# Optimization experiments

Hardware: AMD Instinct MI355X
Metric: run time of the kernel (lower is better)

The kernel has to match this reference:

```python
import jax, jax.numpy as jnp
import numpy as np

N = 100000   # nodes
E = 600000   # edges
B = 512      # graphs in batch
H = 128      # hidden dim
ED = 8       # edge feature dim
TWO48 = float(2 ** 48 - 1)


def _w(k, shape, fan_in):
    return jax.random.normal(k, shape, jnp.float32) * (1.0 / np.sqrt(fan_in))


def setup_inputs() -> dict:
    key = jax.random.key(0)
    ks = jax.random.split(key, 32)
    inp = {}
    inp["s_node_ids"] = jax.random.randint(ks[0], (N,), 0, 2 ** 31 - 1, dtype=jnp.int32)
    inp["s_edge_index"] = jax.random.randint(ks[1], (2, E), 0, N, dtype=jnp.int32)
    inp["s_edge_attr"] = jax.random.normal(ks[2], (E, ED), jnp.float32)
    inp["s_batch"] = jnp.sort(jax.random.randint(ks[3], (N,), 0, B, dtype=jnp.int32))
    inp["depth"] = jax.random.uniform(ks[4], (B,), jnp.float32)
    # id_mlp: Linear(1,H) -> ReLU -> Linear(H,H)
    inp["id_w1"] = _w(ks[5], (1, H), 1); inp["id_b1"] = jnp.zeros((H,), jnp.float32)
    inp["id_w2"] = _w(ks[6], (H, H), H); inp["id_b2"] = jnp.zeros((H,), jnp.float32)
    # edge_mlp: Linear(ED,H) -> ReLU -> Linear(H,H)
    inp["ed_w1"] = _w(ks[7], (ED, H), ED); inp["ed_b1"] = jnp.zeros((H,), jnp.float32)
    inp["ed_w2"] = _w(ks[8], (H, H), H); inp["ed_b2"] = jnp.zeros((H,), jnp.float32)
    # GINEConv nn MLPs: Linear(H,H) -> ReLU -> Linear(H,H)
    inp["c1_w1"] = _w(ks[9], (H, H), H); inp["c1_b1"] = jnp.zeros((H,), jnp.float32)
    inp["c1_w2"] = _w(ks[10], (H, H), H); inp["c1_b2"] = jnp.zeros((H,), jnp.float32)
    inp["c2_w1"] = _w(ks[11], (H, H), H); inp["c2_b1"] = jnp.zeros((H,), jnp.float32)
    inp["c2_w2"] = _w(ks[12], (H, H), H); inp["c2_b2"] = jnp.zeros((H,), jnp.float32)
    inp["rg_w1"] = _w(ks[13], (H + 1, H), H + 1); inp["rg_b1"] = jnp.zeros((H,), jnp.float32)
    inp["rg_w2"] = _w(ks[14], (H, 1), H); inp["rg_b2"] = jnp.zeros((1,), jnp.float32)
    return inp


def _mlp2(x, w1, b1, w2, b2):
    return jax.nn.relu(x @ w1 + b1) @ w2 + b2


def _gine(x, src, dst, e, w1, b1, w2, b2):
    # message = ReLU(x_j + e), sum-aggregated at dst; out = nn((1+eps)*x + aggr), eps=0
    msg = jax.nn.relu(x[src] + e)                       # [E, H]
    aggr = jax.ops.segment_sum(msg, dst, num_segments=N)  # [N, H]
    return _mlp2(x + aggr, w1, b1, w2, b2)


def _global_mean(x, batch):
    sums = jax.ops.segment_sum(x, batch, num_segments=B)                          # [B, H]
    cnts = jax.ops.segment_sum(jnp.ones((x.shape[0], 1), x.dtype), batch, num_segments=B)
    return sums / jnp.maximum(cnts, 1.0)


def reference(s_node_ids, s_edge_index, s_edge_attr, s_batch, depth,
              id_w1, id_b1, id_w2, id_b2,
              ed_w1, ed_b1, ed_w2, ed_b2,
              c1_w1, c1_b1, c1_w2, c1_b2,
              c2_w1, c2_b1, c2_w2, c2_b2,
              rg_w1, rg_b1, rg_w2, rg_b2):
    src, dst = s_edge_index[0], s_edge_index[1]
    x0 = jnp.clip(s_node_ids.astype(jnp.float32) / TWO48, 0.0, 1.0)[:, None]  # [N,1]
    x = _mlp2(x0, id_w1, id_b1, id_w2, id_b2)                                 # [N,H]
    e = _mlp2(s_edge_attr, ed_w1, ed_b1, ed_w2, ed_b2)                        # [E,H]
    x = jax.nn.relu(_gine(x, src, dst, e, c1_w1, c1_b1, c1_w2, c1_b2))
    x = jax.nn.relu(_gine(x, src, dst, e, c2_w1, c2_b1, c2_w2, c2_b2))
    rep = jnp.concatenate([_global_mean(x, s_batch), depth[:, None]], axis=1)  # [B,H+1]
    return _mlp2(rep, rg_w1, rg_b1, rg_w2, rg_b2)[:, 0]                        # [B]
```

## Files before the change

kernel.cpp:

```cpp
#include <hip/hip_runtime.h>
#include <hip/hip_bf16.h>

#define N_NODES 100000
#define N_EDGES 600000
#define NB      512
#define H       128
#define ED      8
#define SCAN_CHUNK 1024
#define N_CHUNKS   98
#define EDGE_BLKS  3125
#define NODE_TILES 1563

typedef __attribute__((ext_vector_type(8))) short short8;
typedef __attribute__((ext_vector_type(4))) float f32x4;
typedef __attribute__((ext_vector_type(4))) unsigned int u32x4;
typedef unsigned short u16;
typedef unsigned int   u32;

static __device__ __forceinline__ u16 f2bf(float f) {
    u32 u = __float_as_uint(f);
    u32 r = u + 0x7fffu + ((u >> 16) & 1u);
    return (u16)(r >> 16);
}
static __device__ __forceinline__ float bf2f(u32 h) {
    return __uint_as_float(h << 16);
}
static __device__ __forceinline__ u32 bfpack(float lo, float hi) {
    u32 r;
    asm("v_cvt_pk_bf16_f32 %0, %1, %2" : "=v"(r) : "v"(lo), "v"(hi));
    return r;
}

__global__ __launch_bounds__(256) void pack_hist_kernel(
    const float* __restrict__ W0, const float* __restrict__ W1,
    const float* __restrict__ W2, const float* __restrict__ W3,
    const float* __restrict__ W4, const float* __restrict__ W5,
    const float* __restrict__ W6,
    short8* __restrict__ O0, short8* __restrict__ O1,
    short8* __restrict__ O2, short8* __restrict__ O3,
    short8* __restrict__ O4, short8* __restrict__ O5,
    short8* __restrict__ O6,
    const int* __restrict__ edge_index, int* __restrict__ counts,
    uint4* __restrict__ sums_zero)
{
    const int HIST_BLKS = (N_EDGES + 255) / 256;
    if (blockIdx.x >= 50 + HIST_BLKS) {
        int idx = (blockIdx.x - 50 - HIST_BLKS) * 256 + threadIdx.x;
        if (idx < 16384) sums_zero[idx] = make_uint4(0, 0, 0, 0);
        return;
    }
    if (blockIdx.x >= 50) {
        int e = (blockIdx.x - 50) * 256 + threadIdx.x;
        if (e < N_EDGES) atomicAdd(&counts[edge_index[N_EDGES + e]], 1);
        return;
    }
    int gid = blockIdx.x * 256 + threadIdx.x;
    const float* W; short8* O; int Krows, kkmax, slot;
    if (gid < 512) { W = W0; O = O0; Krows = ED; kkmax = 1; slot = gid; }
    else {
        int m = (gid - 512) / 2048;
        slot = (gid - 512) % 2048;
        Krows = H; kkmax = 4;
        switch (m) {
            case 0: W = W1; O = O1; break;
            case 1: W = W2; O = O2; break;
            case 2: W = W3; O = O3; break;
            case 3: W = W4; O = O4; break;
            case 4: W = W5; O = O5; break;
            default: W = W6; O = O6; break;
        }
    }
    int lane = slot & 63;
    int t = slot >> 6;
    int nt = t & 1; t >>= 1;
    int kk = t % kkmax;
    int w  = t / kkmax;
    int quad = lane >> 4, n15 = lane & 15;
    int n = w * 32 + nt * 16 + n15;
    short8 v;
    #pragma unroll
    for (int j = 0; j < 8; j++) {
        int k = kk * 32 + quad * 8 + j;
        v[j] = (k < Krows) ? (short)f2bf(W[k * H + n]) : (short)0;
    }
    O[slot] = v;
}

__global__ __launch_bounds__(256) void scan_kernel(
    const int* __restrict__ counts, int* __restrict__ chunk_scan,
    int* __restrict__ bsum_raw)
{
    __shared__ int sS[256];
    int tid = threadIdx.x;
    int base = blockIdx.x * SCAN_CHUNK + tid * 4;
    int4 v = *(const int4*)&counts[base];
    int q0 = v.x, q1 = q0 + v.y, q2 = q1 + v.z, q3 = q2 + v.w;
    sS[tid] = q3;
    __syncthreads();
    #pragma unroll
    for (int off = 1; off < 256; off <<= 1) {
        int t = (tid >= off) ? sS[tid - off] : 0;
        __syncthreads();
        sS[tid] += t;
        __syncthreads();
    }
    int excl = sS[tid] - q3;
    int4 o;
    o.x = excl; o.y = excl + q0; o.z = excl + q1; o.w = excl + q2;
    *(int4*)&chunk_scan[base] = o;
    if (tid == 255) bsum_raw[blockIdx.x] = sS[255];
}

__global__ __launch_bounds__(256) void fill_kernel(
    const int* __restrict__ edge_index,
    const int* __restrict__ chunk_scan, const int* __restrict__ bsum_raw,
    int* __restrict__ counts, int* __restrict__ src_list,
    const float* __restrict__ attr, u16* __restrict__ attr_perm)
{
    __shared__ int sB[128];
    int tid = threadIdx.x;
    int v0 = 0;
    if (tid < 128) {
        v0 = (tid < N_CHUNKS) ? bsum_raw[tid] : 0;
        sB[tid] = v0;
    }
    __syncthreads();
    #pragma unroll
    for (int off = 1; off < 128; off <<= 1) {
        int t = (tid < 128 && tid >= off) ? sB[tid - off] : 0;
        __syncthreads();
        if (tid < 128) sB[tid] += t;
        __syncthreads();
    }
    if (tid < 128) sB[tid] -= v0;
    __syncthreads();

    int e = blockIdx.x * 256 + tid;
    if (e >= N_EDGES) return;
    int src = edge_index[e];
    int dst = edge_index[N_EDGES + e];
    int slot = atomicAdd(&counts[dst], -1) - 1;
    int pos = chunk_scan[dst] + sB[dst >> 10] + slot;
    src_list[pos] = src;
    float4 a0 = *(const float4*)&attr[(long)e * ED];
    float4 a1 = *(const float4*)&attr[(long)e * ED + 4];
    u32 w0 = bfpack(a0.x, a0.y);
    u32 w1 = bfpack(a0.z, a0.w);
    u32 w2 = bfpack(a1.x, a1.y);
    u32 w3 = bfpack(a1.z, a1.w);
    *(uint4*)&attr_perm[(long)pos * ED] = make_uint4(w0, w1, w2, w3);
}

__global__ __launch_bounds__(256) void edge_node_mfma(
    const u16* __restrict__ attr_perm,
    const int* __restrict__ chunk_scan, const int* __restrict__ bsum_raw,
    int* __restrict__ row_start,
    const short8* __restrict__ pW1, const float* __restrict__ b1,
    const short8* __restrict__ pW2, const float* __restrict__ b2,
    u16* __restrict__ e_perm,
    const int* __restrict__ ids,
    const float* __restrict__ id_w1, const float* __restrict__ id_b1,
    const short8* __restrict__ id_pW2, const float* __restrict__ id_b2,
    u16* __restrict__ x_out)
{
    __shared__ u16 sH[64 * 136];
    __shared__ int sB[128];
    __shared__ float s_x0[64];
    int tid = threadIdx.x;

    if (blockIdx.x >= EDGE_BLKS) {
        int tile = blockIdx.x - EDGE_BLKS;
        int w = tid >> 6, lane = tid & 63, quad = lane >> 4, n15 = lane & 15;
        short8 fW2[4][2];
        #pragma unroll
        for (int kk = 0; kk < 4; kk++) {
            fW2[kk][0] = id_pW2[((w * 4 + kk) * 2 + 0) * 64 + lane];
            fW2[kk][1] = id_pW2[((w * 4 + kk) * 2 + 1) * 64 + lane];
        }
        float rb2[2] = { id_b2[w * 32 + n15], id_b2[w * 32 + 16 + n15] };
        float w1c = id_w1[tid & 127], b1c = id_b1[tid & 127];
        int row0 = tile * 64;
        if (tid < 64) {
            int n = row0 + tid;
            float x0 = (n < N_NODES) ? (float)ids[n] / 281474976710655.0f : 0.0f;
            s_x0[tid] = fminf(fmaxf(x0, 0.0f), 1.0f);
        }
        __syncthreads();
        int half = tid >> 7, c = tid & 127;
        #pragma unroll
        for (int rr = 0; rr < 32; rr += 2) {
            int r = half + rr * 2;
            u32 p = bfpack(fmaxf(s_x0[r] * w1c + b1c, 0.0f),
                           fmaxf(s_x0[r + 2] * w1c + b1c, 0.0f));
            sH[r * 136 + c]       = (u16)p;
            sH[(r + 2) * 136 + c] = (u16)(p >> 16);
        }
        __syncthreads();
        f32x4 acc[4][2];
        #pragma unroll
        for (int s = 0; s < 4; s++) { acc[s][0] = (f32x4){0,0,0,0}; acc[s][1] = (f32x4){0,0,0,0}; }
        #pragma unroll
        for (int kk = 0; kk < 4; kk++) {
            #pragma unroll
            for (int s = 0; s < 4; s++) {
                short8 a = *(const short8*)&sH[(s * 16 + n15) * 136 + kk * 32 + quad * 8];
                acc[s][0] = __builtin_amdgcn_mfma_f32_16x16x32_bf16(a, fW2[kk][0], acc[s][0], 0, 0, 0);
                acc[s][1] = __builtin_amdgcn_mfma_f32_16x16x32_bf16(a, fW2[kk][1], acc[s][1], 0, 0, 0);
            }
        }
        __syncthreads();
        #pragma unroll
        for (int s = 0; s < 4; s++)
            #pragma unroll
            for (int nt = 0; nt < 2; nt++) {
                int col = w * 32 + nt * 16 + n15;
                int rb = (s * 16 + quad * 4) * 136 + col;
                u32 p0 = bfpack(acc[s][nt][0] + rb2[nt], acc[s][nt][1] + rb2[nt]);
                u32 p1 = bfpack(acc[s][nt][2] + rb2[nt], acc[s][nt][3] + rb2[nt]);
                sH[rb]       = (u16)p0;
                sH[rb + 136] = (u16)(p0 >> 16);
                sH[rb + 272] = (u16)p1;
                sH[rb + 408] = (u16)(p1 >> 16);
            }
        __syncthreads();
        for (int idx = tid; idx < 64 * 16; idx += 256) {
            int r = idx >> 4, c8 = (idx & 15) << 3;
            int n = row0 + r;
            if (n < N_NODES)
                *(uint4*)&x_out[(long)n * H + c8] = *(const uint4*)&sH[r * 136 + c8];
        }
        return;
    }

    if (blockIdx.x < 392) {
        int v0 = 0;
        if (tid < 128) {
            v0 = (tid < N_CHUNKS) ? bsum_raw[tid] : 0;
            sB[tid] = v0;
        }
        __syncthreads();
        #pragma unroll
        for (int off = 1; off < 128; off <<= 1) {
            int t = (tid < 128 && tid >= off) ? sB[tid - off] : 0;
            __syncthreads();
            if (tid < 128) sB[tid] += t;
            __syncthreads();
        }
        if (tid < 128) sB[tid] -= v0;
        __syncthreads();
        int i = blockIdx.x * 256 + tid;
        if (i <= N_NODES) row_start[i] = chunk_scan[i] + sB[i >> 10];
        __syncthreads();
    }

    int w = tid >> 6, lane = tid & 63, quad = lane >> 4, n15 = lane & 15;
    short8 fW1[2];
    fW1[0] = pW1[(w * 2 + 0) * 64 + lane];
    fW1[1] = pW1[(w * 2 + 1) * 64 + lane];
    short8 fW2[4][2];
    #pragma unroll
    for (int kk = 0; kk < 4; kk++) {
        fW2[kk][0] = pW2[((w * 4 + kk) * 2 + 0) * 64 + lane];
        fW2[kk][1] = pW2[((w * 4 + kk) * 2 + 1) * 64 + lane];
    }
    float rb1[2] = { b1[w * 32 + n15], b1[w * 32 + 16 + n15] };
    float rb2[2] = { b2[w * 32 + n15], b2[w * 32 + 16 + n15] };
    const short8 zero8 = (short8){0,0,0,0,0,0,0,0};
    const int ntile = N_EDGES / 64;
    for (int tile = blockIdx.x; tile < ntile; tile += EDGE_BLKS) {
        int row0 = tile * 64;
        short8 av[4];
        #pragma unroll
        for (int s = 0; s < 4; s++) {
            av[s] = zero8;
            if (quad == 0)
                av[s] = *(const short8*)&attr_perm[(long)(row0 + s * 16 + n15) * ED];
        }
        f32x4 acc[4][2];
        #pragma unroll
        for (int s = 0; s < 4; s++) { acc[s][0] = (f32x4){0,0,0,0}; acc[s][1] = (f32x4){0,0,0,0}; }
        #pragma unroll
        for (int s = 0; s < 4; s++) {
            acc[s][0] = __builtin_amdgcn_mfma_f32_16x16x32_bf16(av[s], fW1[0], acc[s][0], 0, 0, 0);
            acc[s][1] = __builtin_amdgcn_mfma_f32_16x16x32_bf16(av[s], fW1[1], acc[s][1], 0, 0, 0);
        }
        #pragma unroll
        for (int s = 0; s < 4; s++)
            #pragma unroll
            for (int nt = 0; nt < 2; nt++) {
                int col = w * 32 + nt * 16 + n15;
                int rb = (s * 16 + quad * 4) * 136 + col;
                u32 p0 = bfpack(fmaxf(acc[s][nt][0] + rb1[nt], 0.0f),
                                fmaxf(acc[s][nt][1] + rb1[nt], 0.0f));
                u32 p1 = bfpack(fmaxf(acc[s][nt][2] + rb1[nt], 0.0f),
                                fmaxf(acc[s][nt][3] + rb1[nt], 0.0f));
                sH[rb]       = (u16)p0;
                sH[rb + 136] = (u16)(p0 >> 16);
                sH[rb + 272] = (u16)p1;
                sH[rb + 408] = (u16)(p1 >> 16);
            }
        __syncthreads();
        #pragma unroll
        for (int s = 0; s < 4; s++) { acc[s][0] = (f32x4){0,0,0,0}; acc[s][1] = (f32x4){0,0,0,0}; }
        #pragma unroll
        for (int kk = 0; kk < 4; kk++) {
            #pragma unroll
            for (int s = 0; s < 4; s++) {
                short8 a = *(const short8*)&sH[(s * 16 + n15) * 136 + kk * 32 + quad * 8];
                acc[s][0] = __builtin_amdgcn_mfma_f32_16x16x32_bf16(a, fW2[kk][0], acc[s][0], 0, 0, 0);
                acc[s][1] = __builtin_amdgcn_mfma_f32_16x16x32_bf16(a, fW2[kk][1], acc[s][1], 0, 0, 0);
            }
        }
        __syncthreads();
        #pragma unroll
        for (int s = 0; s < 4; s++)
            #pragma unroll
            for (int nt = 0; nt < 2; nt++) {
                int col = w * 32 + nt * 16 + n15;
                int rb = (s * 16 + quad * 4) * 136 + col;
                u32 p0 = bfpack(acc[s][nt][0] + rb2[nt], acc[s][nt][1] + rb2[nt]);
                u32 p1 = bfpack(acc[s][nt][2] + rb2[nt], acc[s][nt][3] + rb2[nt]);
                sH[rb]       = (u16)p0;
                sH[rb + 136] = (u16)(p0 >> 16);
                sH[rb + 272] = (u16)p1;
                sH[rb + 408] = (u16)(p1 >> 16);
            }
        __syncthreads();
        for (int idx = tid; idx < 64 * 16; idx += 256) {
            int r = idx >> 4, c8 = (idx & 15) << 3;
            *(uint4*)&e_perm[(long)(row0 + r) * H + c8] = *(const uint4*)&sH[r * 136 + c8];
        }
        __syncthreads();
    }
}

static __device__ __forceinline__ void acc8(float* a, u32x4 xv, u32x4 ev) {
    #pragma unroll
    for (int q = 0; q < 4; q++) {
        a[2 * q + 0] += fmaxf(bf2f(xv[q] & 0xffff) + bf2f(ev[q] & 0xffff), 0.0f);
        a[2 * q + 1] += fmaxf(bf2f(xv[q] >> 16)    + bf2f(ev[q] >> 16),    0.0f);
    }
}

__global__ __launch_bounds__(256) void gine_fused(
    const int* __restrict__ row_start,
    const int* __restrict__ src_list,
    const u16* __restrict__ e_perm,
    const u16* __restrict__ x,
    const short8* __restrict__ pW1, const float* __restrict__ b1,
    const short8* __restrict__ pW2, const float* __restrict__ b2,
    u16* __restrict__ x_out,
    const int* __restrict__ batch,
    float* __restrict__ sums,
    float* __restrict__ part_sums,
    int* __restrict__ part_id,
    int do_pool)
{
    __shared__ u16 sA[16 * 136];
    __shared__ int sBt[16];
    int tid  = threadIdx.x;
    int lane = tid & 63;
    int l16  = lane & 15;
    int base = lane & 48;
    int fo   = l16 * 8;
    int r    = tid >> 4;
    int n    = blockIdx.x * 16 + r;
    const u16* xb = x + fo;

    if (do_pool && tid < 16) sBt[tid] = batch[blockIdx.x * 16 + tid];

    int beg = row_start[n];
    int end = row_start[n + 1];
    float a[8], b[8];
    #pragma unroll
    for (int q = 0; q < 8; q++) { a[q] = 0.0f; b[q] = 0.0f; }

    for (int j0 = beg; j0 < end; j0 += 16) {
        int m = min(16, end - j0);
        int sv = src_list[j0 + min(l16, m - 1)];
        const u16* ej = e_perm + (long)j0 * H + fo;
        int j = 0;
        for (; j + 2 <= m; j += 2) {
            int s0 = __shfl(sv, base | j);
            int s1 = __shfl(sv, base | (j + 1));
            u32x4 xv0 = *(const u32x4*)(xb + (long)s0 * H);
            u32x4 ev0 = *(const u32x4*)(ej + (long)(j + 0) * H);
            u32x4 xv1 = *(const u32x4*)(xb + (long)s1 * H);
            u32x4 ev1 = *(const u32x4*)(ej + (long)(j + 1) * H);
            acc8(a, xv0, ev0);
            acc8(b, xv1, ev1);
        }
        if (j < m) {
            int s0 = __shfl(sv, base | j);
            u32x4 xv0 = *(const u32x4*)(xb + (long)s0 * H);
            u32x4 ev0 = *(const u32x4*)(ej + (long)j * H);
            acc8(a, xv0, ev0);
        }
    }
    u32x4 xself = *(const u32x4*)(xb + (long)n * H);
    u32x4 xsrow;
    #pragma unroll
    for (int q = 0; q < 4; q++) {
        float o0 = bf2f(xself[q] & 0xffff) + a[2 * q + 0] + b[2 * q + 0];
        float o1 = bf2f(xself[q] >> 16)    + a[2 * q + 1] + b[2 * q + 1];
        xsrow[q] = bfpack(o0, o1);
    }
    *(uint4*)&sA[r * 136 + fo] = *(uint4*)&xsrow;
    __syncthreads();

    int w = tid >> 6, quad = lane >> 4, n15 = l16;
    float rb1[2] = { b1[w * 32 + n15], b1[w * 32 + 16 + n15] };
    float rb2[2] = { b2[w * 32 + n15], b2[w * 32 + 16 + n15] };
    f32x4 acc[2];
    acc[0] = (f32x4){0,0,0,0}; acc[1] = (f32x4){0,0,0,0};
    #pragma unroll
    for (int kk = 0; kk < 4; kk++) {
        short8 av = *(const short8*)&sA[n15 * 136 + kk * 32 + quad * 8];
        short8 w0 = pW1[((w * 4 + kk) * 2 + 0) * 64 + lane];
        short8 w1v = pW1[((w * 4 + kk) * 2 + 1) * 64 + lane];
        acc[0] = __builtin_amdgcn_mfma_f32_16x16x32_bf16(av, w0, acc[0], 0, 0, 0);
        acc[1] = __builtin_amdgcn_mfma_f32_16x16x32_bf16(av, w1v, acc[1], 0, 0, 0);
    }
    __syncthreads();
    #pragma unroll
    for (int nt = 0; nt < 2; nt++) {
        int col = w * 32 + nt * 16 + n15;
        int rb = (quad * 4) * 136 + col;
        u32 p0 = bfpack(fmaxf(acc[nt][0] + rb1[nt], 0.0f),
                        fmaxf(acc[nt][1] + rb1[nt], 0.0f));
        u32 p1 = bfpack(fmaxf(acc[nt][2] + rb1[nt], 0.0f),
                        fmaxf(acc[nt][3] + rb1[nt], 0.0f));
        sA[rb]       = (u16)p0;
        sA[rb + 136] = (u16)(p0 >> 16);
        sA[rb + 272] = (u16)p1;
        sA[rb + 408] = (u16)(p1 >> 16);
    }
    __syncthreads();
    acc[0] = (f32x4){0,0,0,0}; acc[1] = (f32x4){0,0,0,0};
    #pragma unroll
    for (int kk = 0; kk < 4; kk++) {
        short8 av = *(const short8*)&sA[n15 * 136 + kk * 32 + quad * 8];
        short8 w0 = pW2[((w * 4 + kk) * 2 + 0) * 64 + lane];
        short8 w1v = pW2[((w * 4 + kk) * 2 + 1) * 64 + lane];
        acc[0] = __builtin_amdgcn_mfma_f32_16x16x32_bf16(av, w0, acc[0], 0, 0, 0);
        acc[1] = __builtin_amdgcn_mfma_f32_16x16x32_bf16(av, w1v, acc[1], 0, 0, 0);
    }
    __syncthreads();
    #pragma unroll
    for (int nt = 0; nt < 2; nt++) {
        int col = w * 32 + nt * 16 + n15;
        int rb = (quad * 4) * 136 + col;
        u32 p0 = bfpack(fmaxf(acc[nt][0] + rb2[nt], 0.0f),
                        fmaxf(acc[nt][1] + rb2[nt], 0.0f));
        u32 p1 = bfpack(fmaxf(acc[nt][2] + rb2[nt], 0.0f),
                        fmaxf(acc[nt][3] + rb2[nt], 0.0f));
        sA[rb]       = (u16)p0;
        sA[rb + 136] = (u16)(p0 >> 16);
        sA[rb + 272] = (u16)p1;
        sA[rb + 408] = (u16)(p1 >> 16);
    }
    __syncthreads();
    if (!do_pool) {
        int rr = tid >> 4, c8 = (tid & 15) << 3;
        int nn = blockIdx.x * 16 + rr;
        *(uint4*)&x_out[(long)nn * H + c8] = *(const uint4*)&sA[rr * 136 + c8];
    } else {
        if (tid < 64) {
            int c2 = tid * 2;
            float s0 = 0.0f, s1 = 0.0f;
            int cur = sBt[0];
            int seg = 0;
            #pragma unroll
            for (int rr = 0; rr < 16; rr++) {
                int bb = sBt[rr];
                if (bb != cur) {
                    if (seg < 4) {
                        long pb = ((long)blockIdx.x * 4 + seg) * H;
                        part_sums[pb + c2]     = s0;
                        part_sums[pb + c2 + 1] = s1;
                    } else {
                        atomicAdd(&sums[cur * H + c2],     s0);
                        atomicAdd(&sums[cur * H + c2 + 1], s1);
                    }
                    s0 = s1 = 0.0f; cur = bb; seg++;
                }
                u32 v = *(const u32*)&sA[rr * 136 + c2];
                s0 += bf2f(v & 0xffff);
                s1 += bf2f(v >> 16);
            }
            if (seg < 4) {
                long pb = ((long)blockIdx.x * 4 + seg) * H;
                part_sums[pb + c2]     = s0;
                part_sums[pb + c2 + 1] = s1;
            } else {
                atomicAdd(&sums[cur * H + c2],     s0);
                atomicAdd(&sums[cur * H + c2 + 1], s1);
            }
        } else if (tid == 64) {
            int cur = sBt[0];
            int seg = 0;
            #pragma unroll
            for (int rr = 0; rr < 16; rr++) {
                int bb = sBt[rr];
                if (bb != cur) {
                    if (seg < 4) part_id[blockIdx.x * 4 + seg] = cur;
                    cur = bb; seg++;
                }
            }
            if (seg < 4) part_id[blockIdx.x * 4 + seg] = cur;
            for (int s2 = seg + 1; s2 < 4; s2++) part_id[blockIdx.x * 4 + s2] = -1;
        }
    }
}

__global__ __launch_bounds__(128) void regressor_kernel(
    const float* __restrict__ sums,
    const float* __restrict__ part_sums,
    const int* __restrict__ part_id,
    const int* __restrict__ batch,
    const float* __restrict__ depth,
    const float* __restrict__ w1, const float* __restrict__ b1,
    const float* __restrict__ w2, const float* __restrict__ b2,
    float* __restrict__ out)
{
    __shared__ float s_mean[H];
    __shared__ float s_red[2];
    int b = blockIdx.x;
    int j = threadIdx.x;
    int lo = 0, hi = N_NODES;
    while (lo < hi) { int mid = (lo + hi) >> 1; if (batch[mid] < b) lo = mid + 1; else hi = mid; }
    int n_start = lo;
    hi = N_NODES;
    while (lo < hi) { int mid = (lo + hi) >> 1; if (batch[mid] < b + 1) lo = mid + 1; else hi = mid; }
    int n_end = lo;
    float acc = sums[b * H + j];
    if (n_end > n_start) {
        int blk0 = n_start >> 4, blk1 = (n_end - 1) >> 4;
        for (int blk = blk0; blk <= blk1; blk++) {
            #pragma unroll
            for (int s = 0; s < 4; s++)
                if (part_id[blk * 4 + s] == b)
                    acc += part_sums[((long)blk * 4 + s) * H + j];
        }
    }
    float c = fmaxf((float)(n_end - n_start), 1.0f);
    s_mean[j] = acc / c;
    __syncthreads();
    float h = b1[j];
    #pragma unroll 8
    for (int k = 0; k < H; k++) h += s_mean[k] * w1[k * H + j];
    h += depth[b] * w1[H * H + j];
    h = fmaxf(h, 0.0f);
    float p = h * w2[j];
    #pragma unroll
    for (int off = 32; off >= 1; off >>= 1) p += __shfl_down(p, off, 64);
    if ((j & 63) == 0) s_red[j >> 6] = p;
    __syncthreads();
    if (j == 0) out[b] = s_red[0] + s_red[1] + b2[0];
}

extern "C" void kernel_launch(void* const* d_in, const int* in_sizes, int n_in,
                              void* d_out, int out_size, void* d_ws, size_t ws_size,
                              hipStream_t stream)
{
    const int*   ids   = (const int*)  d_in[0];
    const int*   eidx  = (const int*)  d_in[1];
    const float* eattr = (const float*)d_in[2];
    const int*   batch = (const int*)  d_in[3];
    const float* depth = (const float*)d_in[4];
    const float* id_w1 = (const float*)d_in[5];
    const float* id_b1 = (const float*)d_in[6];
    const float* id_w2 = (const float*)d_in[7];
    const float* id_b2 = (const float*)d_in[8];
    const float* ed_w1 = (const float*)d_in[9];
    const float* ed_b1 = (const float*)d_in[10];
    const float* ed_w2 = (const float*)d_in[11];
    const float* ed_b2 = (const float*)d_in[12];
    const float* c1_w1 = (const float*)d_in[13];
    const float* c1_b1 = (const float*)d_in[14];
    const float* c1_w2 = (const float*)d_in[15];
    const float* c1_b2 = (const float*)d_in[16];
    const float* c2_w1 = (const float*)d_in[17];
    const float* c2_b1 = (const float*)d_in[18];
    const float* c2_w2 = (const float*)d_in[19];
    const float* c2_b2 = (const float*)d_in[20];
    const float* rg_w1 = (const float*)d_in[21];
    const float* rg_b1 = (const float*)d_in[22];
    const float* rg_w2 = (const float*)d_in[23];
    const float* rg_b2 = (const float*)d_in[24];

    char* ws = (char*)d_ws;
    u16*   e_buf    = (u16*)  (ws);
    u16*   x_buf    = (u16*)  (ws + 153600000);
    u16*   xs_buf   = (u16*)  (ws + 179200000);
    float* sums_buf = (float*)(ws + 204800000);
    int*   counts   = (int*)  (ws + 205064192);
    int*   chunk_sc = (int*)  (ws + 205465600);
    int*   bsum_raw = (int*)  (ws + 205867008);
    int*   src_list = (int*)  (ws + 205868032);
    short8* ed_w1p  = (short8*)(ws + 208268032);
    short8* ed_w2p  = (short8*)(ws + 208276224);
    short8* c1_w1p  = (short8*)(ws + 208308992);
    short8* c1_w2p  = (short8*)(ws + 208341760);
    short8* c2_w1p  = (short8*)(ws + 208374528);
    short8* c2_w2p  = (short8*)(ws + 208407296);
    short8* id_w2p  = (short8*)(ws + 208440064);
    int*   row_start = counts;
    u16*   attr_perm = xs_buf;
    float* part_sums = (float*)x_buf;
    int*   part_id   = chunk_sc;

    hipMemsetAsync(counts, 0, 401408, stream);

    const int HIST_BLKS = (N_EDGES + 255) / 256;
    pack_hist_kernel<<<50 + HIST_BLKS + 64, 256, 0, stream>>>(
        ed_w1, ed_w2, c1_w1, c1_w2, c2_w1, c2_w2, id_w2,
        ed_w1p, ed_w2p, c1_w1p, c1_w2p, c2_w1p, c2_w2p, id_w2p,
        eidx, counts, (uint4*)sums_buf);

    scan_kernel<<<N_CHUNKS, 256, 0, stream>>>(counts, chunk_sc, bsum_raw);

    fill_kernel<<<(N_EDGES + 255) / 256, 256, 0, stream>>>(
        eidx, chunk_sc, bsum_raw, counts, src_list, eattr, attr_perm);

    edge_node_mfma<<<EDGE_BLKS + NODE_TILES, 256, 0, stream>>>(
        attr_perm, chunk_sc, bsum_raw, row_start,
        ed_w1p, ed_b1, ed_w2p, ed_b2, e_buf,
        ids, id_w1, id_b1, id_w2p, id_b2, x_buf);

    gine_fused<<<6250, 256, 0, stream>>>(row_start, src_list, e_buf, x_buf,
                                         c1_w1p, c1_b1, c1_w2p, c1_b2, xs_buf,
                                         batch, sums_buf, part_sums, part_id, 0);
    gine_fused<<<6250, 256, 0, stream>>>(row_start, src_list, e_buf, xs_buf,
                                         c2_w1p, c2_b1, c2_w2p, c2_b2, x_buf,
                                         batch, sums_buf, part_sums, part_id, 1);

    regressor_kernel<<<NB, 128, 0, stream>>>(sums_buf, part_sums, part_id, batch,
                                             depth, rg_w1, rg_b1, rg_w2, rg_b2,
                                             (float*)d_out);
}
```

Before: 354.7 us.

## Merge CSR build kernels into one cooperative kernel with grid syncs

Replaces the memset, pack/histogram, scan and fill kernels, plus the row_start computation previously done in edge_node_mfma, with a single cooperative kernel of 1024 blocks. The phases are separated by grid-wide syncs and use grid-stride loops. This removes several kernel launches and the launch gaps between them. In exchange it adds grid barrier overhead, leaves fewer blocks for the atomic histogram and fill phases, and moves row_start into a separate buffer.

Result: slower. 712.2 us (+100.8%).

```diff
diff --git a/kernel.cpp b/kernel.cpp
--- a/kernel.cpp
+++ b/kernel.cpp
@@ -1,5 +1,8 @@
 #include <hip/hip_runtime.h>
 #include <hip/hip_bf16.h>
+#include <hip/hip_cooperative_groups.h>
+
+namespace cg = cooperative_groups;
 
 #define N_NODES 100000
 #define N_EDGES 600000
@@ -10,6 +13,7 @@
 #define N_CHUNKS   98
 #define EDGE_BLKS  3125
 #define NODE_TILES 1563
+#define COOP_BLKS  1024
 
 typedef __attribute__((ext_vector_type(8))) short short8;
 typedef __attribute__((ext_vector_type(4))) float f32x4;
@@ -31,7 +35,7 @@
     return r;
 }
 
-__global__ __launch_bounds__(256) void pack_hist_kernel(
+__global__ __launch_bounds__(256) void coop_csr(
     const float* __restrict__ W0, const float* __restrict__ W1,
     const float* __restrict__ W2, const float* __restrict__ W3,
     const float* __restrict__ W4, const float* __restrict__ W5,
@@ -41,84 +45,83 @@
     short8* __restrict__ O4, short8* __restrict__ O5,
     short8* __restrict__ O6,
     const int* __restrict__ edge_index, int* __restrict__ counts,
-    uint4* __restrict__ sums_zero)
+    uint4* __restrict__ sums_zero,
+    int* __restrict__ chunk_scan, int* __restrict__ bsum_raw,
+    int* __restrict__ src_list,
+    const float* __restrict__ attr, u16* __restrict__ attr_perm,
+    int* __restrict__ row_start)
 {
-    const int HIST_BLKS = (N_EDGES + 255) / 256;
-    if (blockIdx.x >= 50 + HIST_BLKS) {
-        int idx = (blockIdx.x - 50 - HIST_BLKS) * 256 + threadIdx.x;
-        if (idx < 16384) sums_zero[idx] = make_uint4(0, 0, 0, 0);
-        return;
-    }
-    if (blockIdx.x >= 50) {
-        int e = (blockIdx.x - 50) * 256 + threadIdx.x;
-        if (e < N_EDGES) atomicAdd(&counts[edge_index[N_EDGES + e]], 1);
-        return;
-    }
-    int gid = blockIdx.x * 256 + threadIdx.x;
-    const float* W; short8* O; int Krows, kkmax, slot;
-    if (gid < 512) { W = W0; O = O0; Krows = ED; kkmax = 1; slot = gid; }
-    else {
-        int m = (gid - 512) / 2048;
-        slot = (gid - 512) % 2048;
-        Krows = H; kkmax = 4;
-        switch (m) {
-            case 0: W = W1; O = O1; break;
-            case 1: W = W2; O = O2; break;
-            case 2: W = W3; O = O3; break;
-            case 3: W = W4; O = O4; break;
-            case 4: W = W5; O = O5; break;
-            default: W = W6; O = O6; break;
-        }
-    }
-    int lane = slot & 63;
-    int t = slot >> 6;
-    int nt = t & 1; t >>= 1;
-    int kk = t % kkmax;
-    int w  = t / kkmax;
-    int quad = lane >> 4, n15 = lane & 15;
-    int n = w * 32 + nt * 16 + n15;
-    short8 v;
-    #pragma unroll
-    for (int j = 0; j < 8; j++) {
-        int k = kk * 32 + quad * 8 + j;
-        v[j] = (k < Krows) ? (short)f2bf(W[k * H + n]) : (short)0;
-    }
-    O[slot] = v;
-}
-
-__global__ __launch_bounds__(256) void scan_kernel(
-    const int* __restrict__ counts, int* __restrict__ chunk_scan,
-    int* __restrict__ bsum_raw)
-{
+    cg::grid_group grid = cg::this_grid();
     __shared__ int sS[256];
-    int tid = threadIdx.x;
-    int base = blockIdx.x * SCAN_CHUNK + tid * 4;
-    int4 v = *(const int4*)&counts[base];
-    int q0 = v.x, q1 = q0 + v.y, q2 = q1 + v.z, q3 = q2 + v.w;
-    sS[tid] = q3;
-    __syncthreads();
-    #pragma unroll
-    for (int off = 1; off < 256; off <<= 1) {
-        int t = (tid >= off) ? sS[tid - off] : 0;
-        __syncthreads();
-        sS[tid] += t;
-        __syncthreads();
-    }
-    int excl = sS[tid] - q3;
-    int4 o;
-    o.x = excl; o.y = excl + q0; o.z = excl + q1; o.w = excl + q2;
-    *(int4*)&chunk_scan[base] = o;
-    if (tid == 255) bsum_raw[blockIdx.x] = sS[255];
-}
-
-__global__ __launch_bounds__(256) void fill_kernel(
-    const int* __restrict__ edge_index,
-    const int* __restrict__ chunk_scan, const int* __restrict__ bsum_raw,
-    int* __restrict__ counts, int* __restrict__ src_list,
-    const float* __restrict__ attr, u16* __restrict__ attr_perm)
-{
     __shared__ int sB[128];
     int tid = threadIdx.x;
+    int bid = blockIdx.x;
+    const int gstride = COOP_BLKS * 256;
+    int gt = bid * 256 + tid;
+
+    if (bid < 50) {
+        int gid = gt;
+        const float* W; short8* O; int Krows, kkmax, slot;
+        if (gid < 512) { W = W0; O = O0; Krows = ED; kkmax = 1; slot = gid; }
+        else {
+            int m = (gid - 512) / 2048;
+            slot = (gid - 512) % 2048;
+            Krows = H; kkmax = 4;
+            switch (m) {
+                case 0: W = W1; O = O1; break;
+                case 1: W = W2; O = O2; break;
+                case 2: W = W3; O = O3; break;
+                case 3: W = W4; O = O4; break;
+                case 4: W = W5; O = O5; break;
+                default: W = W6; O = O6; break;
+            }
+        }
+        int lane = slot & 63;
+        int t = slot >> 6;
+        int nt = t & 1; t >>= 1;
+        int kk = t % kkmax;
+        int w  = t / kkmax;
+        int quad = lane >> 4, n15 = lane & 15;
+        int n = w * 32 + nt * 16 + n15;
+        short8 v;
+        #pragma unroll
+        for (int j = 0; j < 8; j++) {
+            int k = kk * 32 + quad * 8 + j;
+            v[j] = (k < Krows) ? (short)f2bf(W[k * H + n]) : (short)0;
+        }
+        O[slot] = v;
+    }
+    for (int idx = gt; idx < 25088; idx += gstride)
+        ((uint4*)counts)[idx] = make_uint4(0, 0, 0, 0);
+    for (int idx = gt; idx < 16384; idx += gstride)
+        sums_zero[idx] = make_uint4(0, 0, 0, 0);
+    grid.sync();
+
+    for (int e = gt; e < N_EDGES; e += gstride)
+        atomicAdd(&counts[edge_index[N_EDGES + e]], 1);
+    grid.sync();
+
+    if (bid < N_CHUNKS) {
+        int base = bid * SCAN_CHUNK + tid * 4;
+        int4 v = *(const int4*)&counts[base];
+        int q0 = v.x, q1 = q0 + v.y, q2 = q1 + v.z, q3 = q2 + v.w;
+        sS[tid] = q3;
+        __syncthreads();
+        #pragma unroll
+        for (int off = 1; off < 256; off <<= 1) {
+            int t = (tid >= off) ? sS[tid - off] : 0;
+            __syncthreads();
+            sS[tid] += t;
+            __syncthreads();
+        }
+        int excl = sS[tid] - q3;
+        int4 o;
+        o.x = excl; o.y = excl + q0; o.z = excl + q1; o.w = excl + q2;
+        *(int4*)&chunk_scan[base] = o;
+        if (tid == 255) bsum_raw[bid] = sS[255];
+    }
+    grid.sync();
+
     int v0 = 0;
     if (tid < 128) {
         v0 = (tid < N_CHUNKS) ? bsum_raw[tid] : 0;
@@ -135,26 +138,26 @@
     if (tid < 128) sB[tid] -= v0;
     __syncthreads();
 
-    int e = blockIdx.x * 256 + tid;
-    if (e >= N_EDGES) return;
-    int src = edge_index[e];
-    int dst = edge_index[N_EDGES + e];
-    int slot = atomicAdd(&counts[dst], -1) - 1;
-    int pos = chunk_scan[dst] + sB[dst >> 10] + slot;
-    src_list[pos] = src;
-    float4 a0 = *(const float4*)&attr[(long)e * ED];
-    float4 a1 = *(const float4*)&attr[(long)e * ED + 4];
-    u32 w0 = bfpack(a0.x, a0.y);
-    u32 w1 = bfpack(a0.z, a0.w);
-    u32 w2 = bfpack(a1.x, a1.y);
-    u32 w3 = bfpack(a1.z, a1.w);
-    *(uint4*)&attr_perm[(long)pos * ED] = make_uint4(w0, w1, w2, w3);
+    for (int e = gt; e < N_EDGES; e += gstride) {
+        int src = edge_index[e];
+        int dst = edge_index[N_EDGES + e];
+        int slot = atomicAdd(&counts[dst], -1) - 1;
+        int pos = chunk_scan[dst] + sB[dst >> 10] + slot;
+        src_list[pos] = src;
+        float4 a0 = *(const float4*)&attr[(long)e * ED];
+        float4 a1 = *(const float4*)&attr[(long)e * ED + 4];
+        u32 w0 = bfpack(a0.x, a0.y);
+        u32 w1 = bfpack(a0.z, a0.w);
+        u32 w2 = bfpack(a1.x, a1.y);
+        u32 w3 = bfpack(a1.z, a1.w);
+        *(uint4*)&attr_perm[(long)pos * ED] = make_uint4(w0, w1, w2, w3);
+    }
+    for (int i = gt; i <= N_NODES; i += gstride)
+        row_start[i] = chunk_scan[i] + sB[i >> 10];
 }
 
 __global__ __launch_bounds__(256) void edge_node_mfma(
     const u16* __restrict__ attr_perm,
-    const int* __restrict__ chunk_scan, const int* __restrict__ bsum_raw,
-    int* __restrict__ row_start,
     const short8* __restrict__ pW1, const float* __restrict__ b1,
     const short8* __restrict__ pW2, const float* __restrict__ b2,
     u16* __restrict__ e_perm,
@@ -164,7 +167,6 @@
     u16* __restrict__ x_out)
 {
     __shared__ u16 sH[64 * 136];
-    __shared__ int sB[128];
     __shared__ float s_x0[64];
     int tid = threadIdx.x;
 
@@ -230,27 +232,6 @@
                 *(uint4*)&x_out[(long)n * H + c8] = *(const uint4*)&sH[r * 136 + c8];
         }
         return;
-    }
-
-    if (blockIdx.x < 392) {
-        int v0 = 0;
-        if (tid < 128) {
-            v0 = (tid < N_CHUNKS) ? bsum_raw[tid] : 0;
-            sB[tid] = v0;
-        }
-        __syncthreads();
-        #pragma unroll
-        for (int off = 1; off < 128; off <<= 1) {
-            int t = (tid < 128 && tid >= off) ? sB[tid - off] : 0;
-            __syncthreads();
-            if (tid < 128) sB[tid] += t;
-            __syncthreads();
-        }
-        if (tid < 128) sB[tid] -= v0;
-        __syncthreads();
-        int i = blockIdx.x * 256 + tid;
-        if (i <= N_NODES) row_start[i] = chunk_scan[i] + sB[i >> 10];
-        __syncthreads();
     }
 
     int w = tid >> 6, lane = tid & 63, quad = lane >> 4, n15 = lane & 15;
@@ -605,27 +586,25 @@
     short8* c2_w1p  = (short8*)(ws + 208374528);
     short8* c2_w2p  = (short8*)(ws + 208407296);
     short8* id_w2p  = (short8*)(ws + 208440064);
-    int*   row_start = counts;
+    int*   row_start = (int*)  (ws + 208472832);
     u16*   attr_perm = xs_buf;
     float* part_sums = (float*)x_buf;
     int*   part_id   = chunk_sc;
-
-    hipMemsetAsync(counts, 0, 401408, stream);
-
-    const int HIST_BLKS = (N_EDGES + 255) / 256;
-    pack_hist_kernel<<<50 + HIST_BLKS + 64, 256, 0, stream>>>(
-        ed_w1, ed_w2, c1_w1, c1_w2, c2_w1, c2_w2, id_w2,
-        ed_w1p, ed_w2p, c1_w1p, c1_w2p, c2_w1p, c2_w2p, id_w2p,
-        eidx, counts, (uint4*)sums_buf);
-
-    scan_kernel<<<N_CHUNKS, 256, 0, stream>>>(counts, chunk_sc, bsum_raw);
-
-    fill_kernel<<<(N_EDGES + 255) / 256, 256, 0, stream>>>(
-        eidx, chunk_sc, bsum_raw, counts, src_list, eattr, attr_perm);
+    uint4* sums4     = (uint4*)sums_buf;
+
+    void* cargs[] = {
+        (void*)&ed_w1, (void*)&ed_w2, (void*)&c1_w1, (void*)&c1_w2,
+        (void*)&c2_w1, (void*)&c2_w2, (void*)&id_w2,
+        (void*)&ed_w1p, (void*)&ed_w2p, (void*)&c1_w1p, (void*)&c1_w2p,
+        (void*)&c2_w1p, (void*)&c2_w2p, (void*)&id_w2p,
+        (void*)&eidx, (void*)&counts, (void*)&sums4,
+        (void*)&chunk_sc, (void*)&bsum_raw, (void*)&src_list,
+        (void*)&eattr, (void*)&attr_perm, (void*)&row_start };
+    hipLaunchCooperativeKernel((void*)coop_csr, dim3(COOP_BLKS), dim3(256),
+                               cargs, 0, stream);
 
     edge_node_mfma<<<EDGE_BLKS + NODE_TILES, 256, 0, stream>>>(
-        attr_perm, chunk_sc, bsum_raw, row_start,
-        ed_w1p, ed_b1, ed_w2p, ed_b2, e_buf,
+        attr_perm, ed_w1p, ed_b1, ed_w2p, ed_b2, e_buf,
         ids, id_w1, id_b1, id_w2p, id_b2, x_buf);
 
     gine_fused<<<6250, 256, 0, stream>>>(row_start, src_list, e_buf, x_buf,
```
